# Optimization experiments

Hardware: AMD Instinct MI355X
Metric: run time of the kernel (lower is better)

## Reference

```python
import jax, jax.numpy as jnp
import numpy as np

D, L, NH, HD = 384, 12, 6, 64        # embed dim, depth, heads, head dim
H, E, TOPK = 1536, 8, 2              # ffn hidden, experts, top-k
P, IMG, NCLS, B = 16, 224, 1000, 4
NP = (IMG // P) ** 2                 # 196 patches
N = NP + 1                           # +cls


def layer_norm(x, w, b, eps=1e-6):
    m = x.mean(-1, keepdims=True)
    v = jnp.var(x, axis=-1, keepdims=True)
    return (x - m) / jnp.sqrt(v + eps) * w + b


def attention(x, qkv_w, qkv_b, proj_w, proj_b):
    Bx, Nx, C = x.shape
    qkv = (x @ qkv_w.T + qkv_b).reshape(Bx, Nx, 3, NH, HD).transpose(2, 0, 3, 1, 4)
    q, k, v = qkv[0], qkv[1], qkv[2]               # [B,NH,N,HD]
    attn = jax.nn.softmax((q @ k.transpose(0, 1, 3, 2)) * (HD ** -0.5), axis=-1)
    out = (attn @ v).transpose(0, 2, 1, 3).reshape(Bx, Nx, C)
    return out @ proj_w.T + proj_b


def moe_ffn(x, gw, w1, b1, w2, b2):
    # top-k token routing; dense all-expert compute + sparse combine weights
    Bx, Nx, C = x.shape
    t = x.reshape(-1, C)                            # [T,D]
    logits = t @ gw.T                               # [T,E]
    vals, idx = jax.lax.top_k(logits, TOPK)
    w = jax.nn.softmax(vals, axis=-1)               # renormalize over top-k
    combine = jnp.sum(jax.nn.one_hot(idx, E, dtype=t.dtype) * w[..., None], axis=1)  # [T,E]
    h = jax.nn.gelu(jnp.einsum('td,ehd->teh', t, w1) + b1, approximate=False)
    y = jnp.einsum('teh,edh->ted', h, w2) + b2      # [T,E,D]
    return jnp.einsum('te,ted->td', combine, y).reshape(Bx, Nx, C)


def setup_inputs() -> dict:
    key = jax.random.key(0)
    ks = iter(jax.random.split(key, 32))
    s = 0.02
    d = {}
    d['x'] = jax.random.normal(next(ks), (B, 3, IMG, IMG), jnp.float32)
    d['patch_w'] = jax.random.normal(next(ks), (D, 3, P, P)) * s
    d['patch_b'] = jnp.zeros((D,))
    d['cls_token'] = jax.random.normal(next(ks), (1, 1, D)) * s
    d['pos_embed'] = jax.random.normal(next(ks), (1, N, D)) * s
    d['ln1_w'] = jnp.ones((L, D)); d['ln1_b'] = jnp.zeros((L, D))
    d['qkv_w'] = jax.random.normal(next(ks), (L, 3 * D, D)) * s
    d['qkv_b'] = jnp.zeros((L, 3 * D))
    d['proj_w'] = jax.random.normal(next(ks), (L, D, D)) * s
    d['proj_b'] = jnp.zeros((L, D))
    d['ln2_w'] = jnp.ones((L, D)); d['ln2_b'] = jnp.zeros((L, D))
    d['fc1_w'] = jax.random.normal(next(ks), (L // 2, H, D)) * s
    d['fc1_b'] = jnp.zeros((L // 2, H))
    d['fc2_w'] = jax.random.normal(next(ks), (L // 2, D, H)) * s
    d['fc2_b'] = jnp.zeros((L // 2, D))
    d['gate_w'] = jax.random.normal(next(ks), (L // 2, E, D)) * s
    d['e1_w'] = jax.random.normal(next(ks), (L // 2, E, H, D)) * s
    d['e1_b'] = jnp.zeros((L // 2, E, H))
    d['e2_w'] = jax.random.normal(next(ks), (L // 2, E, D, H)) * s
    d['e2_b'] = jnp.zeros((L // 2, E, D))
    d['lnf_w'] = jnp.ones((D,)); d['lnf_b'] = jnp.zeros((D,))
    d['head_w'] = jax.random.normal(next(ks), (NCLS, D)) * s
    d['head_b'] = jnp.zeros((NCLS,))
    return d


def reference(x, patch_w, patch_b, cls_token, pos_embed, ln1_w, ln1_b, qkv_w, qkv_b,
              proj_w, proj_b, ln2_w, ln2_b, fc1_w, fc1_b, fc2_w, fc2_b,
              gate_w, e1_w, e1_b, e2_w, e2_b, lnf_w, lnf_b, head_w, head_b):
    Bx = x.shape[0]
    # patch embed: Conv2d(3, D, kernel=P, stride=P)
    feat = jax.lax.conv_general_dilated(x, patch_w, (P, P), 'VALID',
                                        dimension_numbers=('NCHW', 'OIHW', 'NCHW'))
    t = feat.reshape(Bx, D, NP).transpose(0, 2, 1) + patch_b  # [B,NP,D]
    cls = jnp.broadcast_to(cls_token, (Bx, 1, D))
    h = jnp.concatenate([cls, t], axis=1) + pos_embed          # [B,N,D]
    for l in range(L):
        y = layer_norm(h, ln1_w[l], ln1_b[l])
        h = h + attention(y, qkv_w[l], qkv_b[l], proj_w[l], proj_b[l])
        y = layer_norm(h, ln2_w[l], ln2_b[l])
        m = l // 2
        if l % 2 == 1:  # MoE block
            h = h + moe_ffn(y, gate_w[m], e1_w[m], e1_b[m], e2_w[m], e2_b[m])
        else:           # dense MLP block
            z = jax.nn.gelu(y @ fc1_w[m].T + fc1_b[m], approximate=False)
            h = h + (z @ fc2_w[m].T + fc2_b[m])
    h = layer_norm(h, lnf_w, lnf_b)
    return h[:, 0] @ head_w.T + head_b                         # [B,NCLS]
```

## Files before the change

### kernel.cpp

```cpp
#include <hip/hip_runtime.h>
#include <hip/hip_bf16.h>
#include <math.h>


#define Bv   4
#define Nn   197
#define Tt   788
#define Dd   384
#define Ll   12
#define Hh   1536
#define Ee   8
#define NCLS 1000
#define NPAT 196
#define MPAT (Bv*NPAT)
#define NSLOT (2*Tt)
#define KPAD 224
#define KS   232

#define NQKVW ((size_t)Ll*3*Dd*Dd)
#define NPROJW ((size_t)Ll*Dd*Dd)
#define NFC1W ((size_t)(Ll/2)*Hh*Dd)
#define NFC2W ((size_t)(Ll/2)*Dd*Hh)
#define NE1W  ((size_t)(Ll/2)*Ee*Hh*Dd)
#define NE2W  ((size_t)(Ll/2)*Ee*Dd*Hh)
#define NQKVB ((size_t)Ll*3*Dd)
#define NPROJB ((size_t)Ll*Dd)
#define NFC1B ((size_t)(Ll/2)*Hh)
#define NFC2B ((size_t)(Ll/2)*Dd)
#define NE1B  ((size_t)(Ll/2)*Ee*Hh)
#define NE2B  ((size_t)(Ll/2)*Ee*Dd)

typedef __attribute__((ext_vector_type(8))) short bf16x8;
typedef __attribute__((ext_vector_type(4))) float f32x4;

static __device__ __forceinline__ short f2b(float f) {
    union { __hip_bfloat16 h; short s; } u; u.h = __float2bfloat16(f); return u.s;
}
static __device__ __forceinline__ float b2f_s(short s) {
    union { __hip_bfloat16 h; short s; } u; u.s = s; return __bfloat162float(u.h);
}
static __device__ __forceinline__ float tofl(float v) { return v; }
static __device__ __forceinline__ float tofl(__hip_bfloat16 v) { return __bfloat162float(v); }
static __device__ __forceinline__ float gelu_exact(float v) {
    return 0.5f * v * (1.0f + erff(v * 0.70710678118654752f));
}
static __device__ __forceinline__ bf16x8 load8w(const __hip_bfloat16* p) {
    return *(const bf16x8*)p;
}
static __device__ __forceinline__ bf16x8 load8w(const float* p) {
    const float4* q = (const float4*)p;
    float4 a = q[0], b = q[1];
    bf16x8 r;
    r[0]=f2b(a.x); r[1]=f2b(a.y); r[2]=f2b(a.z); r[3]=f2b(a.w);
    r[4]=f2b(b.x); r[5]=f2b(b.y); r[6]=f2b(b.z); r[7]=f2b(b.w);
    return r;
}
static __device__ __forceinline__ bf16x8 zero8() {
    bf16x8 r;
    #pragma unroll
    for (int i = 0; i < 8; i++) r[i] = 0;
    return r;
}

__global__ void detect_kernel(const void* ln1w, int* flag)
{
    *flag = (*(const unsigned int*)ln1w == 0x3F803F80u) ? 1 : 0;
}

__global__ __launch_bounds__(256)
void cvt_kernel(const void* s0, const void* s1, const void* s2, const void* s3,
                const void* s4, const void* s5, const void* s6, const void* s7,
                const void* s8, const void* s9, const void* s10, const void* s11,
                short* w0, short* w1, short* w2, short* w3, short* w4, short* w5,
                float* f0, float* f1, float* f2, float* f3, float* f4, float* f5,
                const int* flag)
{
    int seg = blockIdx.y;
    const void* src; size_t n; short* dw = nullptr; float* df = nullptr;
    switch (seg) {
        case 0:  src = s0;  n = NQKVW;  dw = w0; break;
        case 1:  src = s1;  n = NPROJW; dw = w1; break;
        case 2:  src = s2;  n = NFC1W;  dw = w2; break;
        case 3:  src = s3;  n = NFC2W;  dw = w3; break;
        case 4:  src = s4;  n = NE1W;   dw = w4; break;
        case 5:  src = s5;  n = NE2W;   dw = w5; break;
        case 6:  src = s6;  n = NQKVB;  df = f0; break;
        case 7:  src = s7;  n = NPROJB; df = f1; break;
        case 8:  src = s8;  n = NFC1B;  df = f2; break;
        case 9:  src = s9;  n = NFC2B;  df = f3; break;
        case 10: src = s10; n = NE1B;   df = f4; break;
        default: src = s11; n = NE2B;   df = f5; break;
    }
    size_t n4 = n >> 2;
    bool isbf = (*flag != 0);
    size_t stride = (size_t)gridDim.x * 256;
    for (size_t i = (size_t)blockIdx.x * 256 + threadIdx.x; i < n4; i += stride) {
        if (dw) {
            if (isbf) {
                ((short4*)dw)[i] = ((const short4*)src)[i];
            } else {
                float4 v = ((const float4*)src)[i];
                short4 o; o.x = f2b(v.x); o.y = f2b(v.y); o.z = f2b(v.z); o.w = f2b(v.w);
                ((short4*)dw)[i] = o;
            }
        } else {
            if (isbf) {
                short4 v = ((const short4*)src)[i];
                float4 o; o.x = b2f_s(v.x); o.y = b2f_s(v.y); o.z = b2f_s(v.z); o.w = b2f_s(v.w);
                ((float4*)df)[i] = o;
            } else {
                ((float4*)df)[i] = ((const float4*)src)[i];
            }
        }
    }
}

template<typename T>
static __device__ void im2col_body(const T* __restrict__ x, short* __restrict__ Pm)
{
    int idx = blockIdx.x * 256 + threadIdx.x;
    if (idx >= MPAT * 768) return;
    int row = idx / 768, col = idx % 768;
    int b = row / NPAT, p = row % NPAT;
    int c = col >> 8, rem = col & 255, i = rem >> 4, j = rem & 15;
    int py = p / 14, px = p % 14;
    Pm[idx] = f2b(tofl(x[(((size_t)b * 3 + c) * 224 + py * 16 + i) * 224 + px * 16 + j]));
}
__global__ __launch_bounds__(256)
void im2col_kernel(const void* x, short* Pm, const int* flag)
{
    if (*flag) im2col_body<__hip_bfloat16>((const __hip_bfloat16*)x, Pm);
    else       im2col_body<float>((const float*)x, Pm);
}

template<typename T>
static __device__ void assemble_body(const float* __restrict__ ptmp, const T* __restrict__ cls,
                                     const T* __restrict__ pos, float* __restrict__ h)
{
    int idx = blockIdx.x * 256 + threadIdx.x;
    if (idx >= Tt * Dd) return;
    int t = idx / Dd, d = idx % Dd;
    int b = t / Nn, n = t % Nn;
    float v = (n == 0) ? tofl(cls[d]) : ptmp[((size_t)b * NPAT + n - 1) * Dd + d];
    h[idx] = v + tofl(pos[(size_t)n * Dd + d]);
}
__global__ __launch_bounds__(256)
void assemble_kernel(const float* ptmp, const void* cls, const void* pos, float* h, const int* flag)
{
    if (*flag) assemble_body<__hip_bfloat16>(ptmp, (const __hip_bfloat16*)cls,
                                             (const __hip_bfloat16*)pos, h);
    else       assemble_body<float>(ptmp, (const float*)cls, (const float*)pos, h);
}

template<typename T>
static __device__ void ln_body(const float* __restrict__ X, const T* __restrict__ w,
                               const T* __restrict__ bb, short* __restrict__ Y16)
{
    int t = blockIdx.x * 4 + (threadIdx.x >> 6);
    int lane = threadIdx.x & 63;
    float v[6], s = 0.f, s2 = 0.f;
    #pragma unroll
    for (int i = 0; i < 6; i++) {
        float xv = X[(size_t)t * Dd + lane + i * 64];
        v[i] = xv; s += xv; s2 += xv * xv;
    }
    #pragma unroll
    for (int off = 32; off > 0; off >>= 1) {
        s  += __shfl_xor(s, off);
        s2 += __shfl_xor(s2, off);
    }
    float mean = s * (1.f / Dd);
    float var  = s2 * (1.f / Dd) - mean * mean;
    float r = rsqrtf(var + 1e-6f);
    #pragma unroll
    for (int i = 0; i < 6; i++) {
        int d = lane + i * 64;
        Y16[(size_t)t * Dd + d] = f2b((v[i] - mean) * r * tofl(w[d]) + tofl(bb[d]));
    }
}
__global__ __launch_bounds__(256)
void ln_kernel(const float* X, const void* w, const void* bb, size_t woff,
               short* Y16, const int* flag)
{
    if (*flag) ln_body<__hip_bfloat16>(X, (const __hip_bfloat16*)w + woff,
                                       (const __hip_bfloat16*)bb + woff, Y16);
    else       ln_body<float>(X, (const float*)w + woff, (const float*)bb + woff, Y16);
}

template<typename WT, int FR>
static __device__ void gemm_body(const short* __restrict__ A, const WT* __restrict__ W,
                                 const WT* __restrict__ bias,
                                 float* __restrict__ Cf, short* __restrict__ Cb,
                                 const float* __restrict__ resid,
                                 int M, int N, int K, int act,
                                 short* lA, short* lB)
{
    int tid = threadIdx.x;
    int m0 = blockIdx.y * (FR * 16), n0 = blockIdx.x * 64;
    int w = tid >> 6, lane = tid & 63, quad = lane >> 4, l15 = lane & 15;
    int arow = tid >> 2, koff = (tid & 3) * 8;
    int gm = m0 + arow;
    f32x4 acc[FR];
    #pragma unroll
    for (int f = 0; f < FR; f++) acc[f] = (f32x4){0.f, 0.f, 0.f, 0.f};

    for (int k0 = 0; k0 < K; k0 += 32) {
        if (arow < FR * 16) {
            bf16x8 av = (gm < M) ? *(const bf16x8*)(A + (size_t)gm * K + k0 + koff) : zero8();
            *(bf16x8*)&lA[arow * 32 + koff] = av;
        }
        *(bf16x8*)&lB[arow * 32 + koff] = load8w(W + (size_t)(n0 + arow) * K + k0 + koff);
        __syncthreads();
        bf16x8 bfrag = *(const bf16x8*)&lB[(w * 16 + l15) * 32 + quad * 8];
        #pragma unroll
        for (int f = 0; f < FR; f++) {
            bf16x8 afrag = *(const bf16x8*)&lA[(f * 16 + l15) * 32 + quad * 8];
            acc[f] = __builtin_amdgcn_mfma_f32_16x16x32_bf16(afrag, bfrag, acc[f], 0, 0, 0);
        }
        __syncthreads();
    }
    int col = n0 + w * 16 + l15;
    float bs = tofl(bias[col]);
    #pragma unroll
    for (int f = 0; f < FR; f++) {
        #pragma unroll
        for (int r = 0; r < 4; r++) {
            int m = m0 + f * 16 + quad * 4 + r;
            if (m >= M) continue;
            float v = acc[f][r] + bs;
            if (act) v = gelu_exact(v);
            if (resid) v += resid[(size_t)m * N + col];
            if (Cf) Cf[(size_t)m * N + col] = v;
            if (Cb) Cb[(size_t)m * N + col] = f2b(v);
        }
    }
}
template<int FR>
__global__ __launch_bounds__(256)
void gemm_kernel(const short* A, const void* W, size_t woff, const void* bias, size_t boff,
                 float* Cf, short* Cb, const float* resid,
                 int M, int N, int K, int act, const int* flag)
{
    __shared__ short lA[FR * 16 * 32];
    __shared__ short lB[64 * 32];
    if (*flag) gemm_body<__hip_bfloat16, FR>(A, (const __hip_bfloat16*)W + woff,
                                             (const __hip_bfloat16*)bias + boff,
                                             Cf, Cb, resid, M, N, K, act, lA, lB);
    else       gemm_body<float, FR>(A, (const float*)W + woff, (const float*)bias + boff,
                                    Cf, Cb, resid, M, N, K, act, lA, lB);
}

template<typename WT>
static __device__ void moe_gemm_body(const short* __restrict__ A, const WT* __restrict__ W,
                                     const WT* __restrict__ bias,
                                     float* __restrict__ Cf, short* __restrict__ Cb,
                                     const int* __restrict__ cnt, const int* __restrict__ perm,
                                     int N, int K, int rshift, int act,
                                     int* rows, short* lA, short* lB)
{
    int e = blockIdx.z;
    int c = cnt[e];
    int r0 = blockIdx.y * 64;
    if (r0 >= c) return;
    int n0 = blockIdx.x * 64;
    int tid = threadIdx.x;
    if (tid < 64) rows[tid] = (r0 + tid < c) ? perm[e * NSLOT + r0 + tid] : -1;
    __syncthreads();
    const WT* We = W + (size_t)e * N * K;
    const WT* be = bias + (size_t)e * N;
    int w = tid >> 6, lane = tid & 63, quad = lane >> 4, l15 = lane & 15;
    int arow = tid >> 2, koff = (tid & 3) * 8;
    int slot = rows[arow];
    f32x4 acc[4];
    #pragma unroll
    for (int f = 0; f < 4; f++) acc[f] = (f32x4){0.f, 0.f, 0.f, 0.f};

    for (int k0 = 0; k0 < K; k0 += 32) {
        bf16x8 av = (slot >= 0) ? *(const bf16x8*)(A + (size_t)(slot >> rshift) * K + k0 + koff)
                                : zero8();
        *(bf16x8*)&lA[arow * 32 + koff] = av;
        *(bf16x8*)&lB[arow * 32 + koff] = load8w(We + (size_t)(n0 + arow) * K + k0 + koff);
        __syncthreads();
        bf16x8 bfrag = *(const bf16x8*)&lB[(w * 16 + l15) * 32 + quad * 8];
        #pragma unroll
        for (int f = 0; f < 4; f++) {
            bf16x8 afrag = *(const bf16x8*)&lA[(f * 16 + l15) * 32 + quad * 8];
            acc[f] = __builtin_amdgcn_mfma_f32_16x16x32_bf16(afrag, bfrag, acc[f], 0, 0, 0);
        }
        __syncthreads();
    }
    int col = n0 + w * 16 + l15;
    float bs = tofl(be[col]);
    #pragma unroll
    for (int f = 0; f < 4; f++) {
        #pragma unroll
        for (int r = 0; r < 4; r++) {
            int s2 = rows[f * 16 + quad * 4 + r];
            if (s2 < 0) continue;
            float v = acc[f][r] + bs;
            if (act) v = gelu_exact(v);
            if (Cf) Cf[(size_t)s2 * N + col] = v;
            if (Cb) Cb[(size_t)s2 * N + col] = f2b(v);
        }
    }
}
__global__ __launch_bounds__(256)
void moe_gemm(const short* A, const void* W, size_t woff, const void* bias, size_t boff,
              float* Cf, short* Cb, const int* cnt, const int* perm,
              int N, int K, int rshift, int act, const int* flag)
{
    __shared__ int rows[64];
    __shared__ short lA[64 * 32];
    __shared__ short lB[64 * 32];
    if (*flag) moe_gemm_body<__hip_bfloat16>(A, (const __hip_bfloat16*)W + woff,
                                             (const __hip_bfloat16*)bias + boff,
                                             Cf, Cb, cnt, perm, N, K, rshift, act, rows, lA, lB);
    else       moe_gemm_body<float>(A, (const float*)W + woff, (const float*)bias + boff,
                                    Cf, Cb, cnt, perm, N, K, rshift, act, rows, lA, lB);
}

template<int FR, int SK>
__global__ __launch_bounds__(256)
void gemm2_kernel(const short* __restrict__ A, const short* __restrict__ W,
                  const float* __restrict__ bias,
                  float* __restrict__ Cf, short* __restrict__ Cb,
                  int M, int N, int K, int act)
{
    constexpr int BUFS = (FR * 16 + 64) * 64;
    constexpr int AIT = FR / 2;
    __shared__ __align__(16) short lds[2 * BUFS];

    const int tid = threadIdx.x;
    const int w = tid >> 6, lane = tid & 63, quad = lane >> 4, l15 = lane & 15;
    const int m0 = blockIdx.y * (FR * 16), n0 = blockIdx.x * 64;
    const int Kp = K / SK;
    const int kb = (SK > 1) ? blockIdx.z * Kp : 0;
    const int nk = Kp >> 6;

    const short* pa[AIT];
    #pragma unroll
    for (int i = 0; i < AIT; i++) {
        int c = tid + i * 256;
        int row = ((c >> 7) << 4) + (c & 15);
        int ck  = (((c >> 6) & 1) << 5) + (((c >> 4) & 3) << 3);
        int gm = m0 + row; if (gm > M - 1) gm = M - 1;
        pa[i] = A + (size_t)gm * K + kb + ck;
    }
    const short* pb[2];
    #pragma unroll
    for (int i = 0; i < 2; i++) {
        int c = tid + i * 256;
        int row = ((c >> 7) << 4) + (c & 15);
        int ck  = (((c >> 6) & 1) << 5) + (((c >> 4) & 3) << 3);
        pb[i] = W + (size_t)(n0 + row) * K + kb + ck;
    }

    f32x4 acc[FR];
    #pragma unroll
    for (int f = 0; f < FR; f++) acc[f] = (f32x4){0.f, 0.f, 0.f, 0.f};

    bf16x8 ra[AIT], rb[2];
    auto loadg = [&](int kt) {
        #pragma unroll
        for (int i = 0; i < AIT; i++) ra[i] = *(const bf16x8*)(pa[i] + kt * 64);
        #pragma unroll
        for (int i = 0; i < 2; i++)  rb[i] = *(const bf16x8*)(pb[i] + kt * 64);
    };
    auto store_lds = [&](int bi) {
        short* bA = lds + bi * BUFS;
        short* bB = bA + FR * 1024;
        #pragma unroll
        for (int i = 0; i < AIT; i++) *(bf16x8*)(bA + (i * 256 + tid) * 8) = ra[i];
        #pragma unroll
        for (int i = 0; i < 2; i++)  *(bf16x8*)(bB + (i * 256 + tid) * 8) = rb[i];
    };
    auto mfma_ph = [&](int bi) {
        const short* bA = lds + bi * BUFS;
        const short* bB = bA + FR * 1024;
        bf16x8 bf[2];
        #pragma unroll
        for (int kk = 0; kk < 2; kk++)
            bf[kk] = *(const bf16x8*)(bB + ((w * 2 + kk) * 64 + lane) * 8);
        #pragma unroll
        for (int f = 0; f < FR; f++) {
            #pragma unroll
            for (int kk = 0; kk < 2; kk++) {
                bf16x8 af = *(const bf16x8*)(bA + ((f * 2 + kk) * 64 + lane) * 8);
                acc[f] = __builtin_amdgcn_mfma_f32_16x16x32_bf16(af, bf[kk], acc[f], 0, 0, 0);
            }
        }
    };

    loadg(0);
    store_lds(0);
    __syncthreads();
    int buf = 0;
    for (int k = 0; k < nk; k++) {
        if (k + 1 < nk) loadg(k + 1);
        mfma_ph(buf);
        if (k + 1 < nk) {
            store_lds(buf ^ 1);
            __syncthreads();
        }
        buf ^= 1;
    }

    const int col = n0 + w * 16 + l15;
    const float bs = bias[col];
    #pragma unroll
    for (int f = 0; f < FR; f++) {
        #pragma unroll
        for (int r = 0; r < 4; r++) {
            int m = m0 + f * 16 + quad * 4 + r;
            if (m >= M) continue;
            float v = acc[f][r];
            if constexpr (SK == 1) {
                v += bs;
                if (act) v = gelu_exact(v);
                if (Cb) Cb[(size_t)m * N + col] = f2b(v);
                if (Cf) Cf[(size_t)m * N + col] = v;
            } else {
                if (blockIdx.z == 0) v += bs;
                atomicAdd(&Cf[(size_t)m * N + col], v);
            }
        }
    }
}

template<int FR>
__global__ __launch_bounds__(256)
void moe2_kernel(const short* __restrict__ A, const short* __restrict__ W,
                 const float* __restrict__ bias,
                 float* __restrict__ Cf, short* __restrict__ Cb,
                 const int* __restrict__ cnt, const int* __restrict__ perm,
                 int N, int K, int rshift, int act)
{
    constexpr int BUFS = (FR * 16 + 64) * 64;
    constexpr int AIT = FR / 2;
    __shared__ __align__(16) short lds[2 * BUFS];
    __shared__ int rows[FR * 16];

    const int e = blockIdx.z;
    const int c0 = cnt[e];
    const int r0 = blockIdx.y * (FR * 16);
    if (r0 >= c0) return;
    const int tid = threadIdx.x;
    if (tid < FR * 16) rows[tid] = (r0 + tid < c0) ? perm[e * NSLOT + r0 + tid] : -1;
    __syncthreads();

    const short* We = W + (size_t)e * N * K;
    const float* be = bias + (size_t)e * N;
    const int w = tid >> 6, lane = tid & 63, quad = lane >> 4, l15 = lane & 15;
    const int n0 = blockIdx.x * 64;
    const int nk = K >> 6;
    const int slot0 = rows[0];

    const short* pa[AIT];
    #pragma unroll
    for (int i = 0; i < AIT; i++) {
        int c = tid + i * 256;
        int row = ((c >> 7) << 4) + (c & 15);
        int ck  = (((c >> 6) & 1) << 5) + (((c >> 4) & 3) << 3);
        int s = rows[row]; if (s < 0) s = slot0;
        pa[i] = A + (size_t)(s >> rshift) * K + ck;
    }
    const short* pb[2];
    #pragma unroll
    for (int i = 0; i < 2; i++) {
        int c = tid + i * 256;
        int row = ((c >> 7) << 4) + (c & 15);
        int ck  = (((c >> 6) & 1) << 5) + (((c >> 4) & 3) << 3);
        pb[i] = We + (size_t)(n0 + row) * K + ck;
    }

    f32x4 acc[FR];
    #pragma unroll
    for (int f = 0; f < FR; f++) acc[f] = (f32x4){0.f, 0.f, 0.f, 0.f};

    bf16x8 ra[AIT], rb[2];
    auto loadg = [&](int kt) {
        #pragma unroll
        for (int i = 0; i < AIT; i++) ra[i] = *(const bf16x8*)(pa[i] + kt * 64);
        #pragma unroll
        for (int i = 0; i < 2; i++)  rb[i] = *(const bf16x8*)(pb[i] + kt * 64);
    };
    auto store_lds = [&](int bi) {
        short* bA = lds + bi * BUFS;
        short* bB = bA + FR * 1024;
        #pragma unroll
        for (int i = 0; i < AIT; i++) *(bf16x8*)(bA + (i * 256 + tid) * 8) = ra[i];
        #pragma unroll
        for (int i = 0; i < 2; i++)  *(bf16x8*)(bB + (i * 256 + tid) * 8) = rb[i];
    };
    auto mfma_ph = [&](int bi) {
        const short* bA = lds + bi * BUFS;
        const short* bB = bA + FR * 1024;
        bf16x8 bf[2];
        #pragma unroll
        for (int kk = 0; kk < 2; kk++)
            bf[kk] = *(const bf16x8*)(bB + ((w * 2 + kk) * 64 + lane) * 8);
        #pragma unroll
        for (int f = 0; f < FR; f++) {
            #pragma unroll
            for (int kk = 0; kk < 2; kk++) {
                bf16x8 af = *(const bf16x8*)(bA + ((f * 2 + kk) * 64 + lane) * 8);
                acc[f] = __builtin_amdgcn_mfma_f32_16x16x32_bf16(af, bf[kk], acc[f], 0, 0, 0);
            }
        }
    };

    loadg(0);
    store_lds(0);
    __syncthreads();
    int buf = 0;
    for (int k = 0; k < nk; k++) {
        if (k + 1 < nk) loadg(k + 1);
        mfma_ph(buf);
        if (k + 1 < nk) {
            store_lds(buf ^ 1);
            __syncthreads();
        }
        buf ^= 1;
    }

    const int col = n0 + w * 16 + l15;
    const float bs = be[col];
    #pragma unroll
    for (int f = 0; f < FR; f++) {
        #pragma unroll
        for (int r = 0; r < 4; r++) {
            int s2 = rows[f * 16 + quad * 4 + r];
            if (s2 < 0) continue;
            float v = acc[f][r] + bs;
            if (act) v = gelu_exact(v);
            if (Cb) Cb[(size_t)s2 * N + col] = f2b(v);
            if (Cf) Cf[(size_t)s2 * N + col] = v;
        }
    }
}

__global__ __launch_bounds__(256)
void attn_kernel(const short* __restrict__ qkv16, short* __restrict__ att16)
{
    __shared__ short lVT[64 * KS];
    __shared__ short lP[4 * 16 * KS];
    int qt = blockIdx.x, hh = blockIdx.y, b = blockIdx.z;
    int tid = threadIdx.x;
    int w = tid >> 6, lane = tid & 63, quad = lane >> 4, l15 = lane & 15;
    const int bq = b * Nn;
    const int rs = 3 * Dd;

    for (int idx = tid; idx < 64 * KPAD; idx += 256) {
        int d = idx & 63, j = idx >> 6;
        short v = (j < Nn) ? qkv16[(size_t)(bq + j) * rs + 2 * Dd + hh * 64 + d] : (short)0;
        lVT[d * KS + j] = v;
    }
    __syncthreads();

    int q0w = qt * 64 + w * 16;
    int qi = q0w + l15;
    size_t qrow = (size_t)(bq + (qi < Nn ? qi : Nn - 1)) * rs + hh * 64;
    bf16x8 a0 = *(const bf16x8*)(qkv16 + qrow + quad * 8);
    bf16x8 a1 = *(const bf16x8*)(qkv16 + qrow + 32 + quad * 8);

    f32x4 sr[13];
    #pragma unroll
    for (int nt = 0; nt < 13; nt++) {
        int key = nt * 16 + l15;
        size_t krow = (size_t)(bq + (key < Nn ? key : Nn - 1)) * rs + Dd + hh * 64;
        bf16x8 b0 = *(const bf16x8*)(qkv16 + krow + quad * 8);
        bf16x8 b1 = *(const bf16x8*)(qkv16 + krow + 32 + quad * 8);
        f32x4 s = (f32x4){0.f, 0.f, 0.f, 0.f};
        s = __builtin_amdgcn_mfma_f32_16x16x32_bf16(a0, b0, s, 0, 0, 0);
        s = __builtin_amdgcn_mfma_f32_16x16x32_bf16(a1, b1, s, 0, 0, 0);
        bool valid = key < Nn;
        #pragma unroll
        for (int r = 0; r < 4; r++) sr[nt][r] = valid ? s[r] * 0.125f : -1e30f;
    }

    float mrow[4], lrow[4], inv[4];
    #pragma unroll
    for (int r = 0; r < 4; r++) {
        float m = -1e30f;
        #pragma unroll
        for (int nt = 0; nt < 13; nt++) m = fmaxf(m, sr[nt][r]);
        #pragma unroll
        for (int off = 1; off < 16; off <<= 1) m = fmaxf(m, __shfl_xor(m, off));
        mrow[r] = m;
        lrow[r] = 0.f;
    }
    #pragma unroll
    for (int nt = 0; nt < 13; nt++) {
        #pragma unroll
        for (int r = 0; r < 4; r++) {
            float ev = expf(sr[nt][r] - mrow[r]);
            lrow[r] += ev;
            lP[(w * 16 + quad * 4 + r) * KS + nt * 16 + l15] = f2b(ev);
        }
    }
    #pragma unroll
    for (int r = 0; r < 4; r++) {
        float s = lrow[r];
        #pragma unroll
        for (int off = 1; off < 16; off <<= 1) s += __shfl_xor(s, off);
        inv[r] = 1.f / s;
        lP[(w * 16 + quad * 4 + r) * KS + 208 + l15] = 0;
    }

    #pragma unroll
    for (int dt = 0; dt < 4; dt++) {
        f32x4 acc = (f32x4){0.f, 0.f, 0.f, 0.f};
        #pragma unroll
        for (int kc = 0; kc < 7; kc++) {
            bf16x8 ap = *(const bf16x8*)&lP[(w * 16 + l15) * KS + kc * 32 + quad * 8];
            bf16x8 bp = *(const bf16x8*)&lVT[(dt * 16 + l15) * KS + kc * 32 + quad * 8];
            acc = __builtin_amdgcn_mfma_f32_16x16x32_bf16(ap, bp, acc, 0, 0, 0);
        }
        #pragma unroll
        for (int r = 0; r < 4; r++) {
            int q = q0w + quad * 4 + r;
            if (q < Nn)
                att16[(size_t)(bq + q) * Dd + hh * 64 + dt * 16 + l15] = f2b(acc[r] * inv[r]);
        }
    }
}

template<typename WT>
static __device__ void gate_body(const short* __restrict__ Y16, const WT* __restrict__ GW,
                                 float* __restrict__ gw_out,
                                 int* __restrict__ cnt, int* __restrict__ perm)
{
    int t = blockIdx.x;
    int lane = threadIdx.x;
    float part[Ee] = {};
    #pragma unroll
    for (int i = 0; i < 6; i++) {
        float yv = b2f_s(Y16[(size_t)t * Dd + lane + i * 64]);
        #pragma unroll
        for (int e = 0; e < Ee; e++)
            part[e] += yv * tofl(GW[(size_t)e * Dd + lane + i * 64]);
    }
    #pragma unroll
    for (int off = 32; off > 0; off >>= 1)
        #pragma unroll
        for (int e = 0; e < Ee; e++) part[e] += __shfl_xor(part[e], off);
    if (lane == 0) {
        int i0 = 0;
        for (int e = 1; e < Ee; e++) if (part[e] > part[i0]) i0 = e;
        int i1 = -1;
        for (int e = 0; e < Ee; e++) {
            if (e == i0) continue;
            if (i1 < 0 || part[e] > part[i1]) i1 = e;
        }
        float e1 = expf(part[i1] - part[i0]);
        float denom = 1.f / (1.f + e1);
        gw_out[t * 2]     = denom;
        gw_out[t * 2 + 1] = e1 * denom;
        int p0 = atomicAdd(&cnt[i0], 1); perm[i0 * NSLOT + p0] = t * 2;
        int p1 = atomicAdd(&cnt[i1], 1); perm[i1 * NSLOT + p1] = t * 2 + 1;
    }
}
__global__ __launch_bounds__(64)
void gate_kernel(const short* Y16, const void* GW, size_t goff, float* gw_out,
                 int* cnt, int* perm, const int* flag)
{
    if (*flag) gate_body<__hip_bfloat16>(Y16, (const __hip_bfloat16*)GW + goff, gw_out, cnt, perm);
    else       gate_body<float>(Y16, (const float*)GW + goff, gw_out, cnt, perm);
}

__global__ __launch_bounds__(256)
void moe_combine(float* __restrict__ h, const float* __restrict__ moeb,
                 const float* __restrict__ gw)
{
    int idx = blockIdx.x * 256 + threadIdx.x;
    if (idx >= Tt * Dd) return;
    int t = idx / Dd, d = idx % Dd;
    h[idx] += gw[t * 2] * moeb[(size_t)(t * 2) * Dd + d]
            + gw[t * 2 + 1] * moeb[(size_t)(t * 2 + 1) * Dd + d];
}

template<typename WT>
static __device__ void head_body(const short* __restrict__ Y16, const WT* __restrict__ hw,
                                 const WT* __restrict__ hb, WT* __restrict__ out)
{
    int idx = blockIdx.x * 256 + threadIdx.x;
    if (idx >= Bv * NCLS) return;
    int b = idx / NCLS, c = idx % NCLS;
    const short* y = Y16 + (size_t)b * Nn * Dd;
    const WT* w = hw + (size_t)c * Dd;
    float acc = 0.f;
    #pragma unroll 8
    for (int k = 0; k < Dd; k++) acc += b2f_s(y[k]) * tofl(w[k]);
    float r = acc + tofl(hb[c]);
    if (sizeof(WT) == 2) { union { __hip_bfloat16 h; WT w2; } u; u.h = __float2bfloat16(r); out[idx] = u.w2; }
    else                 { union { float f; WT w2; } u; u.f = r; out[idx] = u.w2; }
}
__global__ __launch_bounds__(256)
void head_kernel(const short* Y16, const void* hw, const void* hb, void* out, const int* flag)
{
    if (*flag) head_body<__hip_bfloat16>(Y16, (const __hip_bfloat16*)hw, (const __hip_bfloat16*)hb,
                                         (__hip_bfloat16*)out);
    else       head_body<float>(Y16, (const float*)hw, (const float*)hb, (float*)out);
}

extern "C" void kernel_launch(void* const* d_in, const int* in_sizes, int n_in,
                              void* d_out, int out_size, void* d_ws, size_t ws_size,
                              hipStream_t stream)
{
    const void* x       = d_in[0];
    const void* patch_w = d_in[1];
    const void* patch_b = d_in[2];
    const void* cls_tok = d_in[3];
    const void* pos_emb = d_in[4];
    const void* ln1_w   = d_in[5];
    const void* ln1_b   = d_in[6];
    const void* qkv_w   = d_in[7];
    const void* qkv_b   = d_in[8];
    const void* proj_w  = d_in[9];
    const void* proj_b  = d_in[10];
    const void* ln2_w   = d_in[11];
    const void* ln2_b   = d_in[12];
    const void* fc1_w   = d_in[13];
    const void* fc1_b   = d_in[14];
    const void* fc2_w   = d_in[15];
    const void* fc2_b   = d_in[16];
    const void* gate_w  = d_in[17];
    const void* e1_w    = d_in[18];
    const void* e1_b    = d_in[19];
    const void* e2_w    = d_in[20];
    const void* e2_b    = d_in[21];
    const void* lnf_w   = d_in[22];
    const void* lnf_b   = d_in[23];
    const void* head_w  = d_in[24];
    const void* head_b  = d_in[25];

    char* p = (char*)d_ws;
    auto alloc = [&](size_t bytes) { char* r = p; p += (bytes + 255) & ~(size_t)255; return r; };
    float* h     = (float*)alloc((size_t)Tt * Dd * 4);
    short* y16   = (short*)alloc((size_t)Tt * Dd * 2);
    short* qkv16 = (short*)alloc((size_t)Tt * 3 * Dd * 2);
    short* att16 = (short*)alloc((size_t)Tt * Dd * 2);
    short* hid16 = (short*)alloc((size_t)NSLOT * Hh * 2);
    float* moeb  = (float*)alloc((size_t)NSLOT * Dd * 4);
    float* gw    = (float*)alloc((size_t)NSLOT * 4);
    int*   cnt   = (int*)alloc(Ee * 4);
    int*   perm  = (int*)alloc((size_t)Ee * NSLOT * 4);
    int*   flag  = (int*)alloc(4);
    short* Pm    = (short*)alloc((size_t)MPAT * 768 * 2);
    float* ptmp  = (float*)alloc((size_t)MPAT * Dd * 4);
    short* wq  = (short*)alloc(NQKVW * 2);
    short* wp  = (short*)alloc(NPROJW * 2);
    short* w1c = (short*)alloc(NFC1W * 2);
    short* w2c = (short*)alloc(NFC2W * 2);
    short* we1 = (short*)alloc(NE1W * 2);
    short* we2 = (short*)alloc(NE2W * 2);
    float* bq  = (float*)alloc(NQKVB * 4);
    float* bp  = (float*)alloc(NPROJB * 4);
    float* b1c = (float*)alloc(NFC1B * 4);
    float* b2c = (float*)alloc(NFC2B * 4);
    float* be1 = (float*)alloc(NE1B * 4);
    float* be2 = (float*)alloc(NE2B * 4);
    const int use_cvt = ((size_t)(p - (char*)d_ws) <= ws_size);

    dim3 blk(256);
    detect_kernel<<<1, 1, 0, stream>>>(ln1_w, flag);

    if (use_cvt) {
        cvt_kernel<<<dim3(512, 12), blk, 0, stream>>>(
            qkv_w, proj_w, fc1_w, fc2_w, e1_w, e2_w,
            qkv_b, proj_b, fc1_b, fc2_b, e1_b, e2_b,
            wq, wp, w1c, w2c, we1, we2, bq, bp, b1c, b2c, be1, be2, flag);
    }

    im2col_kernel<<<(MPAT * 768 + 255) / 256, blk, 0, stream>>>(x, Pm, flag);
    gemm_kernel<2><<<dim3(Dd / 64, (MPAT + 31) / 32), blk, 0, stream>>>(
        Pm, patch_w, 0, patch_b, 0, ptmp, nullptr, nullptr, MPAT, Dd, 768, 0, flag);
    assemble_kernel<<<(Tt * Dd + 255) / 256, blk, 0, stream>>>(ptmp, cls_tok, pos_emb, h, flag);

    const int MB4 = (Tt + 63) / 64;
    const int MB2 = (Tt + 31) / 32;
    const int MBS = (NSLOT + 63) / 64;
    const int MBS2 = (NSLOT + 31) / 32;

    for (int l = 0; l < Ll; l++) {
        int m = l / 2;
        ln_kernel<<<Tt / 4, blk, 0, stream>>>(h, ln1_w, ln1_b, (size_t)l * Dd, y16, flag);
        if (use_cvt) {
            gemm2_kernel<2, 1><<<dim3(3 * Dd / 64, MB2), blk, 0, stream>>>(
                y16, wq + (size_t)l * 3 * Dd * Dd, bq + (size_t)l * 3 * Dd,
                nullptr, qkv16, Tt, 3 * Dd, Dd, 0);
        } else {
            gemm_kernel<4><<<dim3(3 * Dd / 64, MB4), blk, 0, stream>>>(
                y16, qkv_w, (size_t)l * 3 * Dd * Dd, qkv_b, (size_t)l * 3 * Dd,
                nullptr, qkv16, nullptr, Tt, 3 * Dd, Dd, 0, flag);
        }
        attn_kernel<<<dim3(4, 6, Bv), blk, 0, stream>>>(qkv16, att16);
        if (use_cvt) {
            gemm2_kernel<2, 2><<<dim3(Dd / 64, MB2, 2), blk, 0, stream>>>(
                att16, wp + (size_t)l * Dd * Dd, bp + (size_t)l * Dd,
                h, nullptr, Tt, Dd, Dd, 0);
        } else {
            gemm_kernel<2><<<dim3(Dd / 64, MB2), blk, 0, stream>>>(
                att16, proj_w, (size_t)l * Dd * Dd, proj_b, (size_t)l * Dd,
                h, nullptr, h, Tt, Dd, Dd, 0, flag);
        }
        ln_kernel<<<Tt / 4, blk, 0, stream>>>(h, ln2_w, ln2_b, (size_t)l * Dd, y16, flag);
        if (l % 2 == 0) {
            if (use_cvt) {
                gemm2_kernel<2, 1><<<dim3(Hh / 64, MB2), blk, 0, stream>>>(
                    y16, w1c + (size_t)m * Hh * Dd, b1c + (size_t)m * Hh,
                    nullptr, hid16, Tt, Hh, Dd, 1);
                gemm2_kernel<2, 4><<<dim3(Dd / 64, MB2, 4), blk, 0, stream>>>(
                    hid16, w2c + (size_t)m * Dd * Hh, b2c + (size_t)m * Dd,
                    h, nullptr, Tt, Dd, Hh, 0);
            } else {
                gemm_kernel<4><<<dim3(Hh / 64, MB4), blk, 0, stream>>>(
                    y16, fc1_w, (size_t)m * Hh * Dd, fc1_b, (size_t)m * Hh,
                    nullptr, hid16, nullptr, Tt, Hh, Dd, 1, flag);
                gemm_kernel<2><<<dim3(Dd / 64, MB2), blk, 0, stream>>>(
                    hid16, fc2_w, (size_t)m * Dd * Hh, fc2_b, (size_t)m * Dd,
                    h, nullptr, h, Tt, Dd, Hh, 0, flag);
            }
        } else {
            hipMemsetAsync(cnt, 0, Ee * sizeof(int), stream);
            gate_kernel<<<Tt, 64, 0, stream>>>(
                y16, gate_w, (size_t)m * Ee * Dd, gw, cnt, perm, flag);
            if (use_cvt) {
                moe2_kernel<4><<<dim3(Hh / 64, MBS, Ee), blk, 0, stream>>>(
                    y16, we1 + (size_t)m * Ee * Hh * Dd, be1 + (size_t)m * Ee * Hh,
                    nullptr, hid16, cnt, perm, Hh, Dd, 1, 1);
                moe2_kernel<2><<<dim3(Dd / 64, MBS2, Ee), blk, 0, stream>>>(
                    hid16, we2 + (size_t)m * Ee * Dd * Hh, be2 + (size_t)m * Ee * Dd,
                    moeb, nullptr, cnt, perm, Dd, Hh, 0, 0);
            } else {
                moe_gemm<<<dim3(Hh / 64, MBS, Ee), blk, 0, stream>>>(
                    y16, e1_w, (size_t)m * Ee * Hh * Dd, e1_b, (size_t)m * Ee * Hh,
                    nullptr, hid16, cnt, perm, Hh, Dd, 1, 1, flag);
                moe_gemm<<<dim3(Dd / 64, MBS, Ee), blk, 0, stream>>>(
                    hid16, e2_w, (size_t)m * Ee * Dd * Hh, e2_b, (size_t)m * Ee * Dd,
                    moeb, nullptr, cnt, perm, Dd, Hh, 0, 0, flag);
            }
            moe_combine<<<(Tt * Dd + 255) / 256, blk, 0, stream>>>(h, moeb, gw);
        }
    }

    ln_kernel<<<Tt / 4, blk, 0, stream>>>(h, lnf_w, lnf_b, 0, y16, flag);
    head_kernel<<<(Bv * NCLS + 255) / 256, blk, 0, stream>>>(y16, head_w, head_b, d_out, flag);
}
```

Measured before the change: 1.511 ms.

## Fuse LN with MoE gating, fold combine into expert GEMM, flatten weight conversion

Several independent changes. The weight conversion is merged into one flat grid-stride kernel that also converts the patch-embedding weights, so patch embed can use the pre-converted GEMM path. For MoE layers, LayerNorm and gating are fused, routing is built by a small single-block kernel, and the second expert GEMM accumulates gate-weighted outputs directly into the residual with atomics, removing the memset, the moeb buffer round-trip and the combine kernel. Both GEMM main loops now double-buffer their register prefetch. The final LayerNorm runs only on the CLS tokens. The atomics make float summation order nondeterministic and add register pressure from the extra prefetch registers.

```diff
diff --git a/kernel.cpp b/kernel.cpp
--- a/kernel.cpp
+++ b/kernel.cpp
@@ -23,12 +23,14 @@
 #define NFC2W ((size_t)(Ll/2)*Dd*Hh)
 #define NE1W  ((size_t)(Ll/2)*Ee*Hh*Dd)
 #define NE2W  ((size_t)(Ll/2)*Ee*Dd*Hh)
+#define NPW   ((size_t)Dd*768)
 #define NQKVB ((size_t)Ll*3*Dd)
 #define NPROJB ((size_t)Ll*Dd)
 #define NFC1B ((size_t)(Ll/2)*Hh)
 #define NFC2B ((size_t)(Ll/2)*Dd)
 #define NE1B  ((size_t)(Ll/2)*Ee*Hh)
 #define NE2B  ((size_t)(Ll/2)*Ee*Dd)
+#define NPB   ((size_t)Dd)
 
 typedef __attribute__((ext_vector_type(8))) short bf16x8;
 typedef __attribute__((ext_vector_type(4))) float f32x4;
@@ -67,51 +69,65 @@
     *flag = (*(const unsigned int*)ln1w == 0x3F803F80u) ? 1 : 0;
 }
 
-__global__ __launch_bounds__(256)
-void cvt_kernel(const void* s0, const void* s1, const void* s2, const void* s3,
-                const void* s4, const void* s5, const void* s6, const void* s7,
-                const void* s8, const void* s9, const void* s10, const void* s11,
-                short* w0, short* w1, short* w2, short* w3, short* w4, short* w5,
-                float* f0, float* f1, float* f2, float* f3, float* f4, float* f5,
-                const int* flag)
-{
-    int seg = blockIdx.y;
-    const void* src; size_t n; short* dw = nullptr; float* df = nullptr;
-    switch (seg) {
-        case 0:  src = s0;  n = NQKVW;  dw = w0; break;
-        case 1:  src = s1;  n = NPROJW; dw = w1; break;
-        case 2:  src = s2;  n = NFC1W;  dw = w2; break;
-        case 3:  src = s3;  n = NFC2W;  dw = w3; break;
-        case 4:  src = s4;  n = NE1W;   dw = w4; break;
-        case 5:  src = s5;  n = NE2W;   dw = w5; break;
-        case 6:  src = s6;  n = NQKVB;  df = f0; break;
-        case 7:  src = s7;  n = NPROJB; df = f1; break;
-        case 8:  src = s8;  n = NFC1B;  df = f2; break;
-        case 9:  src = s9;  n = NFC2B;  df = f3; break;
-        case 10: src = s10; n = NE1B;   df = f4; break;
-        default: src = s11; n = NE2B;   df = f5; break;
-    }
-    size_t n4 = n >> 2;
+static __device__ __forceinline__ void cvt_w4(const void* src, short* dst, size_t i, bool isbf) {
+    if (isbf) {
+        ((short4*)dst)[i] = ((const short4*)src)[i];
+    } else {
+        float4 v = ((const float4*)src)[i];
+        short4 o; o.x = f2b(v.x); o.y = f2b(v.y); o.z = f2b(v.z); o.w = f2b(v.w);
+        ((short4*)dst)[i] = o;
+    }
+}
+static __device__ __forceinline__ void cvt_b4(const void* src, float* dst, size_t i, bool isbf) {
+    if (isbf) {
+        short4 v = ((const short4*)src)[i];
+        float4 o; o.x = b2f_s(v.x); o.y = b2f_s(v.y); o.z = b2f_s(v.z); o.w = b2f_s(v.w);
+        ((float4*)dst)[i] = o;
+    } else {
+        ((float4*)dst)[i] = ((const float4*)src)[i];
+    }
+}
+#define CV1  (NQKVW/4)
+#define CV2  (CV1 + NPROJW/4)
+#define CV3  (CV2 + NFC1W/4)
+#define CV4  (CV3 + NFC2W/4)
+#define CV5  (CV4 + NE1W/4)
+#define CV6  (CV5 + NE2W/4)
+#define CV7  (CV6 + NPW/4)
+#define CV8  (CV7 + NQKVB/4)
+#define CV9  (CV8 + NPROJB/4)
+#define CV10 (CV9 + NFC1B/4)
+#define CV11 (CV10 + NFC2B/4)
+#define CV12 (CV11 + NE1B/4)
+#define CV13 (CV12 + NE2B/4)
+#define CVT_TOT (CV13 + NPB/4)
+__global__ __launch_bounds__(256)
+void cvt2_kernel(const void* sq, const void* sp, const void* s1, const void* s2,
+                 const void* se1, const void* se2, const void* spw,
+                 const void* bq_, const void* bp_, const void* b1_, const void* b2_,
+                 const void* be1_, const void* be2_, const void* bpw_,
+                 short* wq, short* wp, short* w1c, short* w2c, short* we1, short* we2,
+                 short* wpc,
+                 float* bq, float* bp, float* b1c, float* b2c, float* be1, float* be2,
+                 float* bpc, const int* flag)
+{
     bool isbf = (*flag != 0);
     size_t stride = (size_t)gridDim.x * 256;
-    for (size_t i = (size_t)blockIdx.x * 256 + threadIdx.x; i < n4; i += stride) {
-        if (dw) {
-            if (isbf) {
-                ((short4*)dw)[i] = ((const short4*)src)[i];
-            } else {
-                float4 v = ((const float4*)src)[i];
-                short4 o; o.x = f2b(v.x); o.y = f2b(v.y); o.z = f2b(v.z); o.w = f2b(v.w);
-                ((short4*)dw)[i] = o;
-            }
-        } else {
-            if (isbf) {
-                short4 v = ((const short4*)src)[i];
-                float4 o; o.x = b2f_s(v.x); o.y = b2f_s(v.y); o.z = b2f_s(v.z); o.w = b2f_s(v.w);
-                ((float4*)df)[i] = o;
-            } else {
-                ((float4*)df)[i] = ((const float4*)src)[i];
-            }
-        }
+    for (size_t i = (size_t)blockIdx.x * 256 + threadIdx.x; i < CVT_TOT; i += stride) {
+        if      (i < CV1)  cvt_w4(sq,  wq,  i,        isbf);
+        else if (i < CV2)  cvt_w4(sp,  wp,  i - CV1,  isbf);
+        else if (i < CV3)  cvt_w4(s1,  w1c, i - CV2,  isbf);
+        else if (i < CV4)  cvt_w4(s2,  w2c, i - CV3,  isbf);
+        else if (i < CV5)  cvt_w4(se1, we1, i - CV4,  isbf);
+        else if (i < CV6)  cvt_w4(se2, we2, i - CV5,  isbf);
+        else if (i < CV7)  cvt_w4(spw, wpc, i - CV6,  isbf);
+        else if (i < CV8)  cvt_b4(bq_, bq,  i - CV7,  isbf);
+        else if (i < CV9)  cvt_b4(bp_, bp,  i - CV8,  isbf);
+        else if (i < CV10) cvt_b4(b1_, b1c, i - CV9,  isbf);
+        else if (i < CV11) cvt_b4(b2_, b2c, i - CV10, isbf);
+        else if (i < CV12) cvt_b4(be1_, be1, i - CV11, isbf);
+        else if (i < CV13) cvt_b4(be2_, be2, i - CV12, isbf);
+        else               cvt_b4(bpw_, bpc, i - CV13, isbf);
     }
 }
 
@@ -185,6 +201,86 @@
     if (*flag) ln_body<__hip_bfloat16>(X, (const __hip_bfloat16*)w + woff,
                                        (const __hip_bfloat16*)bb + woff, Y16);
     else       ln_body<float>(X, (const float*)w + woff, (const float*)bb + woff, Y16);
+}
+
+template<typename T>
+static __device__ void ln_gate_body(const float* __restrict__ X, const T* __restrict__ w,
+                                    const T* __restrict__ bb, short* __restrict__ Y16,
+                                    const T* __restrict__ GW,
+                                    float* __restrict__ gwo, int* __restrict__ sel)
+{
+    int t = blockIdx.x * 4 + (threadIdx.x >> 6);
+    int lane = threadIdx.x & 63;
+    float v[6], s = 0.f, s2 = 0.f;
+    #pragma unroll
+    for (int i = 0; i < 6; i++) {
+        float xv = X[(size_t)t * Dd + lane + i * 64];
+        v[i] = xv; s += xv; s2 += xv * xv;
+    }
+    #pragma unroll
+    for (int off = 32; off > 0; off >>= 1) {
+        s  += __shfl_xor(s, off);
+        s2 += __shfl_xor(s2, off);
+    }
+    float mean = s * (1.f / Dd);
+    float var  = s2 * (1.f / Dd) - mean * mean;
+    float r = rsqrtf(var + 1e-6f);
+    float part[Ee] = {};
+    #pragma unroll
+    for (int i = 0; i < 6; i++) {
+        int d = lane + i * 64;
+        float yv = (v[i] - mean) * r * tofl(w[d]) + tofl(bb[d]);
+        Y16[(size_t)t * Dd + d] = f2b(yv);
+        #pragma unroll
+        for (int e = 0; e < Ee; e++)
+            part[e] += yv * tofl(GW[(size_t)e * Dd + d]);
+    }
+    #pragma unroll
+    for (int off = 32; off > 0; off >>= 1)
+        #pragma unroll
+        for (int e = 0; e < Ee; e++) part[e] += __shfl_xor(part[e], off);
+    if (lane == 0) {
+        int i0 = 0;
+        for (int e = 1; e < Ee; e++) if (part[e] > part[i0]) i0 = e;
+        int i1 = -1;
+        for (int e = 0; e < Ee; e++) {
+            if (e == i0) continue;
+            if (i1 < 0 || part[e] > part[i1]) i1 = e;
+        }
+        float e1 = expf(part[i1] - part[i0]);
+        float denom = 1.f / (1.f + e1);
+        gwo[t * 2]     = denom;
+        gwo[t * 2 + 1] = e1 * denom;
+        sel[t * 2]     = i0;
+        sel[t * 2 + 1] = i1;
+    }
+}
+__global__ __launch_bounds__(256)
+void ln_gate_kernel(const float* X, const void* w, const void* bb, size_t woff,
+                    short* Y16, const void* GW, size_t goff,
+                    float* gwo, int* sel, const int* flag)
+{
+    if (*flag) ln_gate_body<__hip_bfloat16>(X, (const __hip_bfloat16*)w + woff,
+                                            (const __hip_bfloat16*)bb + woff, Y16,
+                                            (const __hip_bfloat16*)GW + goff, gwo, sel);
+    else       ln_gate_body<float>(X, (const float*)w + woff, (const float*)bb + woff, Y16,
+                                   (const float*)GW + goff, gwo, sel);
+}
+
+__global__ __launch_bounds__(256)
+void build_kernel(const int* __restrict__ sel, int* __restrict__ cnt, int* __restrict__ perm)
+{
+    __shared__ int lc[Ee];
+    int tid = threadIdx.x;
+    if (tid < Ee) lc[tid] = 0;
+    __syncthreads();
+    for (int t = tid; t < Tt; t += 256) {
+        int e0 = sel[t * 2], e1 = sel[t * 2 + 1];
+        int p0 = atomicAdd(&lc[e0], 1); perm[e0 * NSLOT + p0] = t * 2;
+        int p1 = atomicAdd(&lc[e1], 1); perm[e1 * NSLOT + p1] = t * 2 + 1;
+    }
+    __syncthreads();
+    if (tid < Ee) cnt[tid] = lc[tid];
 }
 
 template<typename WT, int FR>
@@ -359,14 +455,14 @@
     #pragma unroll
     for (int f = 0; f < FR; f++) acc[f] = (f32x4){0.f, 0.f, 0.f, 0.f};
 
-    bf16x8 ra[AIT], rb[2];
-    auto loadg = [&](int kt) {
-        #pragma unroll
-        for (int i = 0; i < AIT; i++) ra[i] = *(const bf16x8*)(pa[i] + kt * 64);
-        #pragma unroll
-        for (int i = 0; i < 2; i++)  rb[i] = *(const bf16x8*)(pb[i] + kt * 64);
+    bf16x8 raA[AIT], rbA[2], raB[AIT], rbB[2];
+    auto loadg2 = [&](bf16x8 (&ra)[AIT], bf16x8 (&rb)[2], int kt) {
+        #pragma unroll
+        for (int i = 0; i < AIT; i++) ra[i] = *(const bf16x8*)(pa[i] + (size_t)kt * 64);
+        #pragma unroll
+        for (int i = 0; i < 2; i++)  rb[i] = *(const bf16x8*)(pb[i] + (size_t)kt * 64);
     };
-    auto store_lds = [&](int bi) {
+    auto store2 = [&](int bi, bf16x8 (&ra)[AIT], bf16x8 (&rb)[2]) {
         short* bA = lds + bi * BUFS;
         short* bB = bA + FR * 1024;
         #pragma unroll
@@ -391,19 +487,23 @@
         }
     };
 
-    loadg(0);
-    store_lds(0);
+    loadg2(raA, rbA, 0);
+    if (nk > 1) loadg2(raB, rbB, 1);
+    store2(0, raA, rbA);
     __syncthreads();
-    int buf = 0;
-    for (int k = 0; k < nk; k++) {
-        if (k + 1 < nk) loadg(k + 1);
+    int buf = 0, k = 0;
+    for (; k + 1 < nk; k += 2) {
+        if (k + 2 < nk) loadg2(raA, rbA, k + 2);
         mfma_ph(buf);
-        if (k + 1 < nk) {
-            store_lds(buf ^ 1);
-            __syncthreads();
-        }
+        store2(buf ^ 1, raB, rbB);
+        __syncthreads();
         buf ^= 1;
-    }
+        if (k + 3 < nk) loadg2(raB, rbB, k + 3);
+        mfma_ph(buf);
+        if (k + 2 < nk) { store2(buf ^ 1, raA, rbA); __syncthreads(); }
+        buf ^= 1;
+    }
+    if (k < nk) mfma_ph(buf);
 
     const int col = n0 + w * 16 + l15;
     const float bs = bias[col];
@@ -433,7 +533,8 @@
                  const float* __restrict__ bias,
                  float* __restrict__ Cf, short* __restrict__ Cb,
                  const int* __restrict__ cnt, const int* __restrict__ perm,
-                 int N, int K, int rshift, int act)
+                 int N, int K, int rshift, int act,
+                 const float* __restrict__ gw2, float* __restrict__ hcomb)
 {
     constexpr int BUFS = (FR * 16 + 64) * 64;
     constexpr int AIT = FR / 2;
@@ -477,14 +578,14 @@
     #pragma unroll
     for (int f = 0; f < FR; f++) acc[f] = (f32x4){0.f, 0.f, 0.f, 0.f};
 
-    bf16x8 ra[AIT], rb[2];
-    auto loadg = [&](int kt) {
-        #pragma unroll
-        for (int i = 0; i < AIT; i++) ra[i] = *(const bf16x8*)(pa[i] + kt * 64);
-        #pragma unroll
-        for (int i = 0; i < 2; i++)  rb[i] = *(const bf16x8*)(pb[i] + kt * 64);
+    bf16x8 raA[AIT], rbA[2], raB[AIT], rbB[2];
+    auto loadg2 = [&](bf16x8 (&ra)[AIT], bf16x8 (&rb)[2], int kt) {
+        #pragma unroll
+        for (int i = 0; i < AIT; i++) ra[i] = *(const bf16x8*)(pa[i] + (size_t)kt * 64);
+        #pragma unroll
+        for (int i = 0; i < 2; i++)  rb[i] = *(const bf16x8*)(pb[i] + (size_t)kt * 64);
     };
-    auto store_lds = [&](int bi) {
+    auto store2 = [&](int bi, bf16x8 (&ra)[AIT], bf16x8 (&rb)[2]) {
         short* bA = lds + bi * BUFS;
         short* bB = bA + FR * 1024;
         #pragma unroll
@@ -509,19 +610,23 @@
         }
     };
 
-    loadg(0);
-    store_lds(0);
+    loadg2(raA, rbA, 0);
+    if (nk > 1) loadg2(raB, rbB, 1);
+    store2(0, raA, rbA);
     __syncthreads();
-    int buf = 0;
-    for (int k = 0; k < nk; k++) {
-        if (k + 1 < nk) loadg(k + 1);
+    int buf = 0, k = 0;
+    for (; k + 1 < nk; k += 2) {
+        if (k + 2 < nk) loadg2(raA, rbA, k + 2);
         mfma_ph(buf);
-        if (k + 1 < nk) {
-            store_lds(buf ^ 1);
-            __syncthreads();
-        }
+        store2(buf ^ 1, raB, rbB);
+        __syncthreads();
         buf ^= 1;
-    }
+        if (k + 3 < nk) loadg2(raB, rbB, k + 3);
+        mfma_ph(buf);
+        if (k + 2 < nk) { store2(buf ^ 1, raA, rbA); __syncthreads(); }
+        buf ^= 1;
+    }
+    if (k < nk) mfma_ph(buf);
 
     const int col = n0 + w * 16 + l15;
     const float bs = be[col];
@@ -533,8 +638,12 @@
             if (s2 < 0) continue;
             float v = acc[f][r] + bs;
             if (act) v = gelu_exact(v);
-            if (Cb) Cb[(size_t)s2 * N + col] = f2b(v);
-            if (Cf) Cf[(size_t)s2 * N + col] = v;
+            if (gw2) {
+                atomicAdd(&hcomb[(size_t)(s2 >> 1) * N + col], gw2[s2] * v);
+            } else {
+                if (Cb) Cb[(size_t)s2 * N + col] = f2b(v);
+                if (Cf) Cf[(size_t)s2 * N + col] = v;
+            }
         }
     }
 }
@@ -677,6 +786,41 @@
     int t = idx / Dd, d = idx % Dd;
     h[idx] += gw[t * 2] * moeb[(size_t)(t * 2) * Dd + d]
             + gw[t * 2 + 1] * moeb[(size_t)(t * 2 + 1) * Dd + d];
+}
+
+template<typename T>
+static __device__ void lncls_body(const float* __restrict__ X, const T* __restrict__ w,
+                                  const T* __restrict__ bb, short* __restrict__ Y16)
+{
+    int b = threadIdx.x >> 6;
+    int lane = threadIdx.x & 63;
+    size_t t = (size_t)b * Nn;
+    float v[6], s = 0.f, s2 = 0.f;
+    #pragma unroll
+    for (int i = 0; i < 6; i++) {
+        float xv = X[t * Dd + lane + i * 64];
+        v[i] = xv; s += xv; s2 += xv * xv;
+    }
+    #pragma unroll
+    for (int off = 32; off > 0; off >>= 1) {
+        s  += __shfl_xor(s, off);
+        s2 += __shfl_xor(s2, off);
+    }
+    float mean = s * (1.f / Dd);
+    float var  = s2 * (1.f / Dd) - mean * mean;
+    float r = rsqrtf(var + 1e-6f);
+    #pragma unroll
+    for (int i = 0; i < 6; i++) {
+        int d = lane + i * 64;
+        Y16[t * Dd + d] = f2b((v[i] - mean) * r * tofl(w[d]) + tofl(bb[d]));
+    }
+}
+__global__ __launch_bounds__(256)
+void lncls_kernel(const float* X, const void* w, const void* bb, short* Y16, const int* flag)
+{
+    if (*flag) lncls_body<__hip_bfloat16>(X, (const __hip_bfloat16*)w,
+                                          (const __hip_bfloat16*)bb, Y16);
+    else       lncls_body<float>(X, (const float*)w, (const float*)bb, Y16);
 }
 
 template<typename WT>
@@ -745,6 +889,7 @@
     float* gw    = (float*)alloc((size_t)NSLOT * 4);
     int*   cnt   = (int*)alloc(Ee * 4);
     int*   perm  = (int*)alloc((size_t)Ee * NSLOT * 4);
+    int*   sel   = (int*)alloc((size_t)NSLOT * 4);
     int*   flag  = (int*)alloc(4);
     short* Pm    = (short*)alloc((size_t)MPAT * 768 * 2);
     float* ptmp  = (float*)alloc((size_t)MPAT * Dd * 4);
@@ -754,27 +899,35 @@
     short* w2c = (short*)alloc(NFC2W * 2);
     short* we1 = (short*)alloc(NE1W * 2);
     short* we2 = (short*)alloc(NE2W * 2);
+    short* wpc = (short*)alloc(NPW * 2);
     float* bq  = (float*)alloc(NQKVB * 4);
     float* bp  = (float*)alloc(NPROJB * 4);
     float* b1c = (float*)alloc(NFC1B * 4);
     float* b2c = (float*)alloc(NFC2B * 4);
     float* be1 = (float*)alloc(NE1B * 4);
     float* be2 = (float*)alloc(NE2B * 4);
+    float* bpc = (float*)alloc(NPB * 4);
     const int use_cvt = ((size_t)(p - (char*)d_ws) <= ws_size);
 
     dim3 blk(256);
     detect_kernel<<<1, 1, 0, stream>>>(ln1_w, flag);
 
     if (use_cvt) {
-        cvt_kernel<<<dim3(512, 12), blk, 0, stream>>>(
-            qkv_w, proj_w, fc1_w, fc2_w, e1_w, e2_w,
-            qkv_b, proj_b, fc1_b, fc2_b, e1_b, e2_b,
-            wq, wp, w1c, w2c, we1, we2, bq, bp, b1c, b2c, be1, be2, flag);
+        cvt2_kernel<<<4096, blk, 0, stream>>>(
+            qkv_w, proj_w, fc1_w, fc2_w, e1_w, e2_w, patch_w,
+            qkv_b, proj_b, fc1_b, fc2_b, e1_b, e2_b, patch_b,
+            wq, wp, w1c, w2c, we1, we2, wpc,
+            bq, bp, b1c, b2c, be1, be2, bpc, flag);
     }
 
     im2col_kernel<<<(MPAT * 768 + 255) / 256, blk, 0, stream>>>(x, Pm, flag);
-    gemm_kernel<2><<<dim3(Dd / 64, (MPAT + 31) / 32), blk, 0, stream>>>(
-        Pm, patch_w, 0, patch_b, 0, ptmp, nullptr, nullptr, MPAT, Dd, 768, 0, flag);
+    if (use_cvt) {
+        gemm2_kernel<2, 1><<<dim3(Dd / 64, (MPAT + 31) / 32), blk, 0, stream>>>(
+            Pm, wpc, bpc, ptmp, nullptr, MPAT, Dd, 768, 0);
+    } else {
+        gemm_kernel<2><<<dim3(Dd / 64, (MPAT + 31) / 32), blk, 0, stream>>>(
+            Pm, patch_w, 0, patch_b, 0, ptmp, nullptr, nullptr, MPAT, Dd, 768, 0, flag);
+    }
     assemble_kernel<<<(Tt * Dd + 255) / 256, blk, 0, stream>>>(ptmp, cls_tok, pos_emb, h, flag);
 
     const int MB4 = (Tt + 63) / 64;
@@ -804,8 +957,8 @@
                 att16, proj_w, (size_t)l * Dd * Dd, proj_b, (size_t)l * Dd,
                 h, nullptr, h, Tt, Dd, Dd, 0, flag);
         }
-        ln_kernel<<<Tt / 4, blk, 0, stream>>>(h, ln2_w, ln2_b, (size_t)l * Dd, y16, flag);
         if (l % 2 == 0) {
+            ln_kernel<<<Tt / 4, blk, 0, stream>>>(h, ln2_w, ln2_b, (size_t)l * Dd, y16, flag);
             if (use_cvt) {
                 gemm2_kernel<2, 1><<<dim3(Hh / 64, MB2), blk, 0, stream>>>(
                     y16, w1c + (size_t)m * Hh * Dd, b1c + (size_t)m * Hh,
@@ -822,28 +975,37 @@
                     h, nullptr, h, Tt, Dd, Hh, 0, flag);
             }
         } else {
-            hipMemsetAsync(cnt, 0, Ee * sizeof(int), stream);
-            gate_kernel<<<Tt, 64, 0, stream>>>(
-                y16, gate_w, (size_t)m * Ee * Dd, gw, cnt, perm, flag);
             if (use_cvt) {
+                ln_gate_kernel<<<Tt / 4, blk, 0, stream>>>(
+                    h, ln2_w, ln2_b, (size_t)l * Dd, y16,
+                    gate_w, (size_t)m * Ee * Dd, gw, sel, flag);
+                build_kernel<<<1, blk, 0, stream>>>(sel, cnt, perm);
                 moe2_kernel<4><<<dim3(Hh / 64, MBS, Ee), blk, 0, stream>>>(
                     y16, we1 + (size_t)m * Ee * Hh * Dd, be1 + (size_t)m * Ee * Hh,
-                    nullptr, hid16, cnt, perm, Hh, Dd, 1, 1);
+                    nullptr, hid16, cnt, perm, Hh, Dd, 1, 1, nullptr, nullptr);
                 moe2_kernel<2><<<dim3(Dd / 64, MBS2, Ee), blk, 0, stream>>>(
                     hid16, we2 + (size_t)m * Ee * Dd * Hh, be2 + (size_t)m * Ee * Dd,
-                    moeb, nullptr, cnt, perm, Dd, Hh, 0, 0);
+                    nullptr, nullptr, cnt, perm, Dd, Hh, 0, 0, gw, h);
             } else {
+                ln_kernel<<<Tt / 4, blk, 0, stream>>>(h, ln2_w, ln2_b, (size_t)l * Dd, y16, flag);
+                hipMemsetAsync(cnt, 0, Ee * sizeof(int), stream);
+                gate_kernel<<<Tt, 64, 0, stream>>>(
+                    y16, gate_w, (size_t)m * Ee * Dd, gw, cnt, perm, flag);
                 moe_gemm<<<dim3(Hh / 64, MBS, Ee), blk, 0, stream>>>(
                     y16, e1_w, (size_t)m * Ee * Hh * Dd, e1_b, (size_t)m * Ee * Hh,
                     nullptr, hid16, cnt, perm, Hh, Dd, 1, 1, flag);
                 moe_gemm<<<dim3(Dd / 64, MBS, Ee), blk, 0, stream>>>(
                     hid16, e2_w, (size_t)m * Ee * Dd * Hh, e2_b, (size_t)m * Ee * Dd,
                     moeb, nullptr, cnt, perm, Dd, Hh, 0, 0, flag);
+                moe_combine<<<(Tt * Dd + 255) / 256, blk, 0, stream>>>(h, moeb, gw);
             }
-            moe_combine<<<(Tt * Dd + 255) / 256, blk, 0, stream>>>(h, moeb, gw);
-        }
-    }
-
-    ln_kernel<<<Tt / 4, blk, 0, stream>>>(h, lnf_w, lnf_b, 0, y16, flag);
+        }
+    }
+
+    if (use_cvt) {
+        lncls_kernel<<<1, blk, 0, stream>>>(h, lnf_w, lnf_b, y16, flag);
+    } else {
+        ln_kernel<<<Tt / 4, blk, 0, stream>>>(h, lnf_w, lnf_b, 0, y16, flag);
+    }
     head_kernel<<<(Bv * NCLS + 255) / 256, blk, 0, stream>>>(y16, head_w, head_b, d_out, flag);
 }
```

New measurement: 1.398 ms. 7.5% less time.
